# Performance work log

Hardware: AMD Instinct MI355X
Metric: run time of the kernel (lower is better)

## Reference

```python
import jax, jax.numpy as jnp
import numpy as np

B = 64
C = 12        # num_classes
NC = 16       # num_clusters
N0, N1, N2, N3, NDIM = 2048, 1000, 500, 100, 3
E = C * NC    # 192 residual heads


def _init(key, shape, fan_in):
    return jax.random.normal(key, shape, dtype=jnp.float32) / np.sqrt(fan_in)


def setup_inputs() -> dict:
    key = jax.random.key(0)
    ks = jax.random.split(key, 12)
    x = jax.random.normal(ks[0], (B, N0), dtype=jnp.float32)
    class_label = jax.random.randint(ks[1], (B, 1), 0, C)
    return {
        'x': x,
        'class_label': class_label,
        # bin_3layer weights, stacked over the class axis
        'W1b': _init(ks[2], (C, N1, N0), N0),
        'b1b': jnp.zeros((C, N1), jnp.float32),
        'W2b': _init(ks[3], (C, N2, N1), N1),
        'b2b': jnp.zeros((C, N2), jnp.float32),
        'W3b': _init(ks[4], (C, NC, N2), N2),
        'b3b': jnp.zeros((C, NC), jnp.float32),
        # res_2layer weights, stacked over class*cluster axis
        'W1r': _init(ks[5], (E, N3, N0), N0),
        'b1r': jnp.zeros((E, N3), jnp.float32),
        'W2r': _init(ks[6], (E, NDIM, N3), N3),
        'b2r': jnp.zeros((E, NDIM), jnp.float32),
    }


def reference(x, class_label, W1b, b1b, W2b, b2b, W3b, b3b, W1r, b1r, W2r, b2r):
    # --- bin heads: all classes computed (as the torch loop does), grouped GEMMs ---
    h = jax.nn.relu(jnp.einsum('bi,cji->bcj', x, W1b) + b1b)        # [B,C,N1]
    h = jax.nn.relu(jnp.einsum('bcj,ckj->bck', h, W2b) + b2b)       # [B,C,N2]
    y1_all = jnp.einsum('bck,cmk->bcm', h, W3b) + b3b               # [B,C,NC]

    # --- res heads: all class*cluster experts computed ---
    r = jax.nn.relu(jnp.einsum('bi,eji->bej', x, W1r) + b1r)        # [B,E,N3]
    y2_all = jnp.einsum('bej,edj->bed', r, W2r) + b2r               # [B,E,NDIM]
    y2_all = y2_all.reshape(B, C, NC, NDIM)

    # one-hot bmm over class axis == gather per-sample class
    cl = class_label[:, 0]                                           # [B]
    y1 = jnp.take_along_axis(y1_all, cl[:, None, None], axis=1)[:, 0]        # [B,NC]
    y2c = jnp.take_along_axis(y2_all, cl[:, None, None, None], axis=1)[:, 0] # [B,NC,NDIM]

    # argmax over clusters, then one-hot bmm over cluster axis == gather
    pose = jnp.argmax(y1, axis=1)                                    # [B]
    y2 = jnp.take_along_axis(y2c, pose[:, None, None], axis=1)[:, 0] # [B,NDIM]
    return y1, y2
```

## Files before the change

kernel.cpp:

```cpp
#include <hip/hip_runtime.h>

#define B_   64
#define C_   12
#define NC_  16
#define N0_  2048
#define N1_  1000
#define N2_  500
#define N3_  100

__device__ __forceinline__ float wred(float v) {
#pragma unroll
    for (int off = 32; off > 0; off >>= 1) v += __shfl_xor(v, off, 64);
    return v;
}

__global__ __launch_bounds__(256)
void k_l1b(const float* __restrict__ x, const int* __restrict__ cls,
           const float* __restrict__ W1b, const float* __restrict__ b1b,
           float* __restrict__ h1) {
    const int lane = threadIdx.x & 63;
    const int wave = threadIdx.x >> 6;
    const int t    = blockIdx.x * 4 + wave;
    const int c    = t % C_;
    const int j0   = (t / C_) * 2;

    const unsigned long long m = __ballot(cls[lane] == c);
    if (m == 0ull) return;

    const float4* wr0 = (const float4*)(W1b + ((size_t)c * N1_ + j0) * N0_);
    const float4* wr1 = wr0 + (N0_ / 4);
    float4 w0[8], w1[8];
#pragma unroll
    for (int f = 0; f < 8; ++f) { w0[f] = wr0[f * 64 + lane]; w1[f] = wr1[f * 64 + lane]; }
    const float bias0 = b1b[c * N1_ + j0];
    const float bias1 = b1b[c * N1_ + j0 + 1];

    for (unsigned long long mm = m; mm; mm &= (mm - 1ull)) {
        const int b = (int)__builtin_ctzll(mm);
        const float4* xr = (const float4*)(x + (size_t)b * N0_);
        float a0 = 0.f, a1 = 0.f;
#pragma unroll
        for (int f = 0; f < 8; ++f) {
            const float4 xv = xr[f * 64 + lane];
            a0 += w0[f].x * xv.x + w0[f].y * xv.y + w0[f].z * xv.z + w0[f].w * xv.w;
            a1 += w1[f].x * xv.x + w1[f].y * xv.y + w1[f].z * xv.z + w1[f].w * xv.w;
        }
        const float s0 = wred(a0), s1 = wred(a1);
        if (lane == 0) {
            h1[(size_t)b * N1_ + j0]     = fmaxf(s0 + bias0, 0.f);
            h1[(size_t)b * N1_ + j0 + 1] = fmaxf(s1 + bias1, 0.f);
        }
    }
}

__global__ __launch_bounds__(1024)
void k_perb(const float* __restrict__ x, const int* __restrict__ cls,
            const float* __restrict__ h1,
            const float* __restrict__ W2b, const float* __restrict__ b2b,
            const float* __restrict__ W3b, const float* __restrict__ b3b,
            const float* __restrict__ W1r, const float* __restrict__ b1r,
            const float* __restrict__ W2r, const float* __restrict__ b2r,
            float* __restrict__ out_y1, float* __restrict__ out_y2) {
    const int b    = blockIdx.x;
    const int tid  = threadIdx.x;
    const int lane = tid & 63;
    const int wave = tid >> 6;
    const int c    = cls[b];

    __shared__ __align__(16) float s_x[N0_];
    __shared__ __align__(16) float s_h1[N1_];
    __shared__ float s_h2[N2_];
    __shared__ float s_y1[NC_];
    __shared__ float s_r[N3_];
    __shared__ int   s_e;

    for (int i = tid; i < N0_; i += 1024) s_x[i]  = x[(size_t)b * N0_ + i];
    for (int i = tid; i < N1_; i += 1024) s_h1[i] = h1[(size_t)b * N1_ + i];
    __syncthreads();

    {
        const float4* xr = (const float4*)s_h1;
        for (int j0 = wave * 2; j0 < N2_; j0 += 32) {
            const float4* wr0 = (const float4*)(W2b + ((size_t)c * N2_ + j0) * N1_);
            const float4* wr1 = wr0 + (N1_ / 4);
            float a0 = 0.f, a1 = 0.f;
#pragma unroll
            for (int f = 0; f < 4; ++f) {
                const int idx = f * 64 + lane;
                if (idx < N1_ / 4) {
                    const float4 xv = xr[idx];
                    const float4 w0 = wr0[idx], w1 = wr1[idx];
                    a0 += w0.x * xv.x + w0.y * xv.y + w0.z * xv.z + w0.w * xv.w;
                    a1 += w1.x * xv.x + w1.y * xv.y + w1.z * xv.z + w1.w * xv.w;
                }
            }
            const float s0 = wred(a0), s1 = wred(a1);
            if (lane == 0) {
                s_h2[j0]     = fmaxf(s0 + b2b[c * N2_ + j0],     0.f);
                s_h2[j0 + 1] = fmaxf(s1 + b2b[c * N2_ + j0 + 1], 0.f);
            }
        }
    }
    __syncthreads();

    if (wave < NC_) {
        const float* wrow = W3b + ((size_t)c * NC_ + wave) * N2_;
        float a = 0.f;
        for (int k = lane; k < N2_; k += 64) a += s_h2[k] * wrow[k];
        const float s = wred(a) + b3b[c * NC_ + wave];
        if (lane == 0) { s_y1[wave] = s; out_y1[b * NC_ + wave] = s; }
    }
    __syncthreads();

    if (wave == 0) {
        float v  = (lane < NC_) ? s_y1[lane] : -1e30f;
        int   mi = lane;
#pragma unroll
        for (int off = 8; off > 0; off >>= 1) {
            const float ov = __shfl_xor(v,  off, 16);
            const int   om = __shfl_xor(mi, off, 16);
            if (ov > v || (ov == v && om < mi)) { v = ov; mi = om; }
        }
        if (lane == 0) s_e = c * NC_ + mi;
    }
    __syncthreads();
    const int e = s_e;

    {
        const float4* xr = (const float4*)s_x;
        for (int j0 = wave * 2; j0 < N3_; j0 += 32) {
            const float4* wr0 = (const float4*)(W1r + ((size_t)e * N3_ + j0) * N0_);
            const float4* wr1 = wr0 + (N0_ / 4);
            float a0 = 0.f, a1 = 0.f;
#pragma unroll
            for (int f = 0; f < 8; ++f) {
                const int idx = f * 64 + lane;
                const float4 xv = xr[idx];
                const float4 w0 = wr0[idx], w1 = wr1[idx];
                a0 += w0.x * xv.x + w0.y * xv.y + w0.z * xv.z + w0.w * xv.w;
                a1 += w1.x * xv.x + w1.y * xv.y + w1.z * xv.z + w1.w * xv.w;
            }
            const float s0 = wred(a0), s1 = wred(a1);
            if (lane == 0) {
                s_r[j0]     = fmaxf(s0 + b1r[e * N3_ + j0],     0.f);
                s_r[j0 + 1] = fmaxf(s1 + b1r[e * N3_ + j0 + 1], 0.f);
            }
        }
    }
    __syncthreads();

    if (wave < 3) {
        const float* w2 = W2r + ((size_t)e * 3 + wave) * N3_;
        float a = s_r[lane] * w2[lane];
        if (lane < N3_ - 64) a += s_r[64 + lane] * w2[64 + lane];
        const float s = wred(a);
        if (lane == 0) out_y2[b * 3 + wave] = s + b2r[e * 3 + wave];
    }
}

extern "C" void kernel_launch(void* const* d_in, const int* in_sizes, int n_in,
                              void* d_out, int out_size, void* d_ws, size_t ws_size,
                              hipStream_t stream) {
    const float* x   = (const float*)d_in[0];
    const int*   cls = (const int*)  d_in[1];
    const float* W1b = (const float*)d_in[2];
    const float* b1b = (const float*)d_in[3];
    const float* W2b = (const float*)d_in[4];
    const float* b2b = (const float*)d_in[5];
    const float* W3b = (const float*)d_in[6];
    const float* b3b = (const float*)d_in[7];
    const float* W1r = (const float*)d_in[8];
    const float* b1r = (const float*)d_in[9];
    const float* W2r = (const float*)d_in[10];
    const float* b2r = (const float*)d_in[11];

    float* out_y1 = (float*)d_out;
    float* out_y2 = (float*)d_out + B_ * NC_;
    float* h1     = (float*)d_ws;

    hipLaunchKernelGGL(k_l1b, dim3(1500), dim3(256), 0, stream,
                       x, cls, W1b, b1b, h1);
    hipLaunchKernelGGL(k_perb, dim3(64), dim3(1024), 0, stream,
                       x, cls, h1, W2b, b2b, W3b, b3b, W1r, b1r, W2r, b2r,
                       out_y1, out_y2);
}
```

Baseline: 68.88 us.

## Fuse layer-1 and per-sample kernels into one persistent kernel with grid barrier

Merges the two launches into a single 256-block kernel. Every block first computes a slice of the layer-1 bin-head tasks, then increments an atomic counter. The first 64 blocks spin on that counter before reading h1 and running the per-sample tail. A small zeroing kernel resets the counter each call. This is meant to hide the second kernel's launch gap and overlap loading x with the layer-1 work. It relies on all 256 blocks being co-resident, which at 1024 threads each needs at least one block per CU; if that does not hold the spin-wait can deadlock.

```diff
diff --git a/kernel.cpp b/kernel.cpp
--- a/kernel.cpp
+++ b/kernel.cpp
@@ -7,6 +7,9 @@
 #define N1_  1000
 #define N2_  500
 #define N3_  100
+#define AGENT __HIP_MEMORY_SCOPE_AGENT
+#define NBLK  256
+#define TASKS (C_ * (N1_ / 2))
 
 __device__ __forceinline__ float wred(float v) {
 #pragma unroll
@@ -14,58 +17,66 @@
     return v;
 }
 
-__global__ __launch_bounds__(256)
-void k_l1b(const float* __restrict__ x, const int* __restrict__ cls,
+__global__ void k_zero(int* __restrict__ z) {
+    if (threadIdx.x < 16) z[threadIdx.x] = 0;
+}
+
+__global__ __launch_bounds__(1024)
+void k_all(const float* __restrict__ x, const int* __restrict__ cls,
            const float* __restrict__ W1b, const float* __restrict__ b1b,
-           float* __restrict__ h1) {
-    const int lane = threadIdx.x & 63;
-    const int wave = threadIdx.x >> 6;
-    const int t    = blockIdx.x * 4 + wave;
-    const int c    = t % C_;
-    const int j0   = (t / C_) * 2;
-
-    const unsigned long long m = __ballot(cls[lane] == c);
-    if (m == 0ull) return;
-
-    const float4* wr0 = (const float4*)(W1b + ((size_t)c * N1_ + j0) * N0_);
-    const float4* wr1 = wr0 + (N0_ / 4);
-    float4 w0[8], w1[8];
-#pragma unroll
-    for (int f = 0; f < 8; ++f) { w0[f] = wr0[f * 64 + lane]; w1[f] = wr1[f * 64 + lane]; }
-    const float bias0 = b1b[c * N1_ + j0];
-    const float bias1 = b1b[c * N1_ + j0 + 1];
-
-    for (unsigned long long mm = m; mm; mm &= (mm - 1ull)) {
-        const int b = (int)__builtin_ctzll(mm);
-        const float4* xr = (const float4*)(x + (size_t)b * N0_);
-        float a0 = 0.f, a1 = 0.f;
-#pragma unroll
-        for (int f = 0; f < 8; ++f) {
-            const float4 xv = xr[f * 64 + lane];
-            a0 += w0[f].x * xv.x + w0[f].y * xv.y + w0[f].z * xv.z + w0[f].w * xv.w;
-            a1 += w1[f].x * xv.x + w1[f].y * xv.y + w1[f].z * xv.z + w1[f].w * xv.w;
-        }
-        const float s0 = wred(a0), s1 = wred(a1);
-        if (lane == 0) {
-            h1[(size_t)b * N1_ + j0]     = fmaxf(s0 + bias0, 0.f);
-            h1[(size_t)b * N1_ + j0 + 1] = fmaxf(s1 + bias1, 0.f);
-        }
-    }
-}
-
-__global__ __launch_bounds__(1024)
-void k_perb(const float* __restrict__ x, const int* __restrict__ cls,
-            const float* __restrict__ h1,
-            const float* __restrict__ W2b, const float* __restrict__ b2b,
-            const float* __restrict__ W3b, const float* __restrict__ b3b,
-            const float* __restrict__ W1r, const float* __restrict__ b1r,
-            const float* __restrict__ W2r, const float* __restrict__ b2r,
-            float* __restrict__ out_y1, float* __restrict__ out_y2) {
-    const int b    = blockIdx.x;
+           const float* __restrict__ W2b, const float* __restrict__ b2b,
+           const float* __restrict__ W3b, const float* __restrict__ b3b,
+           const float* __restrict__ W1r, const float* __restrict__ b1r,
+           const float* __restrict__ W2r, const float* __restrict__ b2r,
+           float* __restrict__ h1, int* __restrict__ doneA,
+           float* __restrict__ out_y1, float* __restrict__ out_y2) {
     const int tid  = threadIdx.x;
     const int lane = tid & 63;
     const int wave = tid >> 6;
-    const int c    = cls[b];
+    const int cls_lane = cls[lane];
+
+    {
+        const int start = (blockIdx.x * TASKS) >> 8;
+        const int end   = ((blockIdx.x + 1) * TASKS) >> 8;
+        for (int t = start + wave; t < end; t += 16) {
+            const int c  = t % C_;
+            const int j0 = (t / C_) * 2;
+            const unsigned long long m = __ballot(cls_lane == c);
+            if (m == 0ull) continue;
+            const float4* wr0 = (const float4*)(W1b + ((size_t)c * N1_ + j0) * N0_);
+            const float4* wr1 = wr0 + (N0_ / 4);
+            float4 w0[8], w1[8];
+#pragma unroll
+            for (int f = 0; f < 8; ++f) { w0[f] = wr0[f * 64 + lane]; w1[f] = wr1[f * 64 + lane]; }
+            const float bias0 = b1b[c * N1_ + j0];
+            const float bias1 = b1b[c * N1_ + j0 + 1];
+            for (unsigned long long mm = m; mm; mm &= (mm - 1ull)) {
+                const int bb = (int)__builtin_ctzll(mm);
+                const float4* xr = (const float4*)(x + (size_t)bb * N0_);
+                float a0 = 0.f, a1 = 0.f;
+#pragma unroll
+                for (int f = 0; f < 8; ++f) {
+                    const float4 xv = xr[f * 64 + lane];
+                    a0 += w0[f].x * xv.x + w0[f].y * xv.y + w0[f].z * xv.z + w0[f].w * xv.w;
+                    a1 += w1[f].x * xv.x + w1[f].y * xv.y + w1[f].z * xv.z + w1[f].w * xv.w;
+                }
+                const float s0 = wred(a0), s1 = wred(a1);
+                if (lane == 0) {
+                    h1[(size_t)bb * N1_ + j0]     = fmaxf(s0 + bias0, 0.f);
+                    h1[(size_t)bb * N1_ + j0 + 1] = fmaxf(s1 + bias1, 0.f);
+                }
+            }
+        }
+    }
+    __syncthreads();
+    if (tid == 0) {
+        __threadfence();
+        __hip_atomic_fetch_add(doneA, 1, __ATOMIC_ACQ_REL, AGENT);
+    }
+    if (blockIdx.x >= B_) return;
+
+    const int b = blockIdx.x;
+    const int c = cls[b];
 
     __shared__ __align__(16) float s_x[N0_];
     __shared__ __align__(16) float s_h1[N1_];
@@ -74,8 +85,15 @@
     __shared__ float s_r[N3_];
     __shared__ int   s_e;
 
-    for (int i = tid; i < N0_; i += 1024) s_x[i]  = x[(size_t)b * N0_ + i];
-    for (int i = tid; i < N1_; i += 1024) s_h1[i] = h1[(size_t)b * N1_ + i];
+    if (tid < 512) ((float4*)s_x)[tid] = ((const float4*)(x + (size_t)b * N0_))[tid];
+
+    if (tid == 0) {
+        while (__hip_atomic_load(doneA, __ATOMIC_RELAXED, AGENT) < NBLK)
+            __builtin_amdgcn_s_sleep(2);
+        __hip_atomic_fetch_add(doneA, 0, __ATOMIC_ACQ_REL, AGENT);
+    }
+    __syncthreads();
+    if (tid < 250) ((float4*)s_h1)[tid] = ((const float4*)(h1 + (size_t)b * N1_))[tid];
     __syncthreads();
 
     {
@@ -176,11 +194,13 @@
 
     float* out_y1 = (float*)d_out;
     float* out_y2 = (float*)d_out + B_ * NC_;
-    float* h1     = (float*)d_ws;
-
-    hipLaunchKernelGGL(k_l1b, dim3(1500), dim3(256), 0, stream,
-                       x, cls, W1b, b1b, h1);
-    hipLaunchKernelGGL(k_perb, dim3(64), dim3(1024), 0, stream,
-                       x, cls, h1, W2b, b2b, W3b, b3b, W1r, b1r, W2r, b2r,
-                       out_y1, out_y2);
-}
+
+    char*  ws    = (char*)d_ws;
+    float* h1    = (float*)(ws);
+    int*   doneA = (int*)  (ws + 256000);
+
+    hipLaunchKernelGGL(k_zero, dim3(1), dim3(64), 0, stream, doneA);
+    hipLaunchKernelGGL(k_all, dim3(NBLK), dim3(1024), 0, stream,
+                       x, cls, W1b, b1b, W2b, b2b, W3b, b3b, W1r, b1r, W2r, b2r,
+                       h1, doneA, out_y1, out_y2);
+}
```

After: 98.39 us. 42.9% more time.
